# Kernel optimization log

Hardware: AMD Instinct MI355X
Metric: run time of the kernel (lower is better)

Reference implementation:

```python
import jax, jax.numpy as jnp
import numpy as np

OBS_DIM, ACTION_DIM, H, FC = 64, 100, 512, 256
IN_DIM = FC + ACTION_DIM


def setup_inputs() -> dict:
    key = jax.random.key(0)
    ks = jax.random.split(key, 10)
    s = lambda k, shp, fan: jax.random.normal(k, shp, jnp.float32) * (1.0 / np.sqrt(fan))
    return {
        "observations": jax.random.normal(ks[0], (32, 2048, OBS_DIM), jnp.float32),
        "actions": jax.random.uniform(ks[1], (32, 2048), jnp.float32),
        "W_obs": s(ks[2], (OBS_DIM, FC), OBS_DIM), "b_obs": jnp.zeros((FC,), jnp.float32),
        "W_act": s(ks[3], (1, ACTION_DIM), 1), "b_act": jnp.zeros((ACTION_DIM,), jnp.float32),
        "W_lstm": s(ks[4], (IN_DIM, 4 * H), IN_DIM),
        "U_lstm": s(ks[5], (H, 4 * H), H),
        "b_lstm": jnp.zeros((4 * H,), jnp.float32),
        "W_proj": s(ks[6], (H, ACTION_DIM), H), "b_proj": jnp.zeros((ACTION_DIM,), jnp.float32),
    }


def _lstm_seq(x, W, U, b):
    # x: [B, T, D] -> outputs [B, T, H]; keras LSTMCell default activations.
    B = x.shape[0]
    h0 = jnp.zeros((B, H), x.dtype)
    c0 = jnp.zeros((B, H), x.dtype)

    def step(carry, x_t):
        h, c = carry
        z = x_t @ W + h @ U + b  # [B, 4H]
        i, f, g, o = jnp.split(z, 4, axis=-1)
        i = jax.nn.sigmoid(i); f = jax.nn.sigmoid(f)
        g = jnp.tanh(g); o = jax.nn.sigmoid(o)
        c = f * c + i * g
        h = o * jnp.tanh(c)
        return (h, c), h

    _, hs = jax.lax.scan(step, (h0, c0), jnp.swapaxes(x, 0, 1))  # [T, B, H]
    return jnp.swapaxes(hs, 0, 1)


def reference(observations, actions, W_obs, b_obs, W_act, b_act,
              W_lstm, U_lstm, b_lstm, W_proj, b_proj):
    a = jax.nn.relu(actions[..., None] @ W_act + b_act)        # [B, T, A]
    ob = jax.nn.relu(observations @ W_obs + b_obs)             # [B, T, FC]
    x = jnp.concatenate([ob, a], axis=-1)                      # [B, T, FC+A]
    seq = _lstm_seq(x, W_lstm, U_lstm, b_lstm)                 # [B, T, H]
    logits = seq @ W_proj + b_proj                             # [B, T, A]
    pi = jax.nn.softmax(logits, axis=-1)
    # tf.math.argmax(logits) defaults to axis=0 (over batch), kept faithfully.
    argmax_actions = jnp.argmax(logits, axis=0)
    return pi, logits, argmax_actions
```

## Files before the change

### kernel.cpp

```cpp
#include <hip/hip_runtime.h>
#include <cstdint>
#include <cstddef>

#define B_   32
#define T_   2048
#define OBS_ 64
#define FC_  256
#define ACT_ 100
#define H_   512
#define TC_  128
#define NCH_ 16

typedef __attribute__((ext_vector_type(4))) unsigned int u32x4;
typedef __attribute__((ext_vector_type(8))) short bf16x8;
typedef __attribute__((ext_vector_type(4))) float f32x4;

static __device__ __forceinline__ bf16x8 as_b(u32x4 v){ union{u32x4 u; bf16x8 b;} x; x.u=v; return x.b; }
static __device__ __forceinline__ unsigned short f2bf(float f){
  unsigned int u = __builtin_bit_cast(unsigned int, f);
  return (unsigned short)((u + 0x7fffu + ((u>>16)&1u)) >> 16);
}
static __device__ __forceinline__ float bf2f(unsigned short s){
  unsigned int u = ((unsigned int)s) << 16;
  return __builtin_bit_cast(float, u);
}
static __device__ __forceinline__ void split3(float v, unsigned short& h, unsigned short& m, unsigned short& l){
  h = f2bf(v);
  float r1 = v - bf2f(h);
  m = f2bf(r1);
  float r2 = r1 - bf2f(m);
  l = f2bf(r2);
}
static __device__ __forceinline__ u32x4 pack8(const unsigned short* v){
  u32x4 r;
  r.x = (unsigned)v[0] | ((unsigned)v[1]<<16);
  r.y = (unsigned)v[2] | ((unsigned)v[3]<<16);
  r.z = (unsigned)v[4] | ((unsigned)v[5]<<16);
  r.w = (unsigned)v[6] | ((unsigned)v[7]<<16);
  return r;
}
static __device__ __forceinline__ u32x4 load_cohx4(const unsigned int* p){
  u32x4 r;
  asm volatile("global_load_dwordx4 %0, %1, off sc0 sc1"
               : "=&v"(r) : "v"(p) : "memory");
  return r;
}

static constexpr size_t XF_OFF    = 0;
static constexpr size_t XF_SZ     = (size_t)TC_*2*12*3*64*16;
static constexpr size_t WF_OFF    = XF_OFF + XF_SZ;
static constexpr size_t WF_SZ     = (size_t)32*4*28*3*64*16;
static constexpr size_t WPF_OFF   = WF_OFF + WF_SZ;
static constexpr size_t WPF_SZ    = (size_t)7*16*3*64*16;
static constexpr size_t ZX_OFF    = WPF_OFF + WPF_SZ;
static constexpr size_t ZX_SZ     = (size_t)TC_*2*2048*16*4;
static constexpr size_t HC01_OFF  = ZX_OFF + ZX_SZ;
static constexpr size_t HC01_SZ   = (size_t)TC_*2*16*512*4;
static constexpr size_t HC2_OFF   = HC01_OFF + HC01_SZ;
static constexpr size_t HC2_SZ    = (size_t)TC_*2*16*512*2;
static constexpr size_t HG_OFF    = HC2_OFF + HC2_SZ;
static constexpr size_t HG_SZ     = (size_t)3*2*16*2*256*4;
static constexpr size_t CST_OFF   = HG_OFF + HG_SZ;
static constexpr size_t CST_SZ    = (size_t)B_*H_*4;
static constexpr size_t CTR_OFF   = CST_OFF + CST_SZ;
static constexpr size_t CTR_SZ    = (size_t)2*T_*4;

__global__ __launch_bounds__(256) void k_prep_x(
    const float* __restrict__ obs, const float* __restrict__ act,
    const float* __restrict__ Wobs, const float* __restrict__ bobs,
    const float* __restrict__ Wact, const float* __restrict__ bact,
    u32x4* __restrict__ Xf, int tbase)
{
  __shared__ float Wl[64][257];
  __shared__ float ol[32][64];
  __shared__ float xr[32][256];
  __shared__ float al[32];
  __shared__ float wal[100], bal[100], bol[256];
  int tl = blockIdx.x; int t = tbase + tl; int tid = threadIdx.x;
  for (int i = tid; i < 64*256; i += 256) Wl[i>>8][i&255] = Wobs[i];
  for (int i = tid; i < 32*64; i += 256)
    ol[i>>6][i&63] = obs[((size_t)(i>>6)*T_ + t)*OBS_ + (i&63)];
  if (tid < 32) al[tid] = act[(size_t)tid*T_ + t];
  if (tid < 100) { wal[tid] = Wact[tid]; bal[tid] = bact[tid]; }
  bol[tid] = bobs[tid];
  __syncthreads();
  {
    int k = tid;
    double accd[32];
#pragma unroll
    for (int r = 0; r < 32; ++r) accd[r] = 0.0;
    for (int kc = 0; kc < 64; kc += 8) {
      float w[8];
#pragma unroll
      for (int q = 0; q < 8; ++q) w[q] = Wl[kc+q][k];
#pragma unroll
      for (int r = 0; r < 32; ++r) {
#pragma unroll
        for (int q = 0; q < 8; ++q) accd[r] += (double)w[q]*(double)ol[r][kc+q];
      }
    }
#pragma unroll
    for (int r = 0; r < 32; ++r) xr[r][k] = fmaxf((float)(accd[r] + (double)bol[k]), 0.f);
  }
  __syncthreads();
  int g = tid >> 6, l = tid & 63;
  int r = l & 15, sub = l >> 4;
  for (int p = g; p < 24; p += 4) {
    int bg = p / 12, kk = p % 12;
    int b = bg*16 + r;
    unsigned short vh[8], vm[8], vl[8];
#pragma unroll
    for (int j = 0; j < 8; ++j) {
      int k = kk*32 + sub*8 + j;
      float x;
      if (k < 256)      x = xr[b][k];
      else if (k < 356) {
        double tmp = (double)al[b]*(double)wal[k-256] + (double)bal[k-256];
        x = fmaxf((float)tmp, 0.f);
      } else            x = 0.f;
      split3(x, vh[j], vm[j], vl[j]);
    }
    size_t base = ((((size_t)tl*2 + bg)*12 + kk)*3)*64 + l;
    Xf[base]       = pack8(vh);
    Xf[base + 64]  = pack8(vm);
    Xf[base + 128] = pack8(vl);
  }
}

__global__ __launch_bounds__(256) void k_prep_w(
    const float* __restrict__ Wl, const float* __restrict__ Ul,
    unsigned short* __restrict__ Wf)
{
  size_t gid = (size_t)blockIdx.x*256 + threadIdx.x;
  if (gid >= (size_t)896*2048) return;
  int k = (int)(gid >> 11), oc = (int)(gid & 2047);
  float v = 0.f;
  if (k < 356) v = Wl[(size_t)k*2048 + oc];
  else if (k >= 384) v = Ul[(size_t)(k-384)*2048 + oc];
  unsigned short vh, vm, vlo;
  split3(v, vh, vm, vlo);
  int g = oc >> 9, hu = oc & 511;
  int hs = hu >> 4, wv = (hu >> 2) & 3, u = hu & 3;
  int cc = g*4 + u;
  int kk = k >> 5, sub = (k >> 3) & 3, j = k & 7;
  size_t e = ((((size_t)(hs*4 + wv)*28 + kk)*3 + 0)*64 + (sub*16 + cc))*8 + j;
  Wf[e]        = vh;
  Wf[e + 512]  = vm;
  Wf[e + 1024] = vlo;
}

__global__ __launch_bounds__(256) void k_prep_wp(
    const float* __restrict__ Wp, unsigned short* __restrict__ Wpf)
{
  int gid = blockIdx.x*256 + threadIdx.x;
  if (gid >= 512*112) return;
  int k = gid / 112, c = gid % 112;
  float v = (c < 100) ? Wp[(size_t)k*100 + c] : 0.f;
  unsigned short vh, vm, vlo;
  split3(v, vh, vm, vlo);
  int ct = c >> 4, cl = c & 15;
  int kk = k >> 5, sub = (k >> 3) & 3, j = k & 7;
  size_t e = (((size_t)(ct*16 + kk)*3 + 0)*64 + (sub*16 + cl))*8 + j;
  Wpf[e]        = vh;
  Wpf[e + 512]  = vm;
  Wpf[e + 1024] = vlo;
}

__global__ __launch_bounds__(256) void k_prep_zx(
    const u32x4* __restrict__ Xf, const u32x4* __restrict__ Wf,
    const float* __restrict__ blstm, float* __restrict__ zxT)
{
  int bid = blockIdx.x;
  int hq = bid & 7, bg = (bid >> 3) & 1, tl = bid >> 4;
  int tid = threadIdx.x;
  int v = tid >> 6, lane = tid & 63;
  int cc = lane & 15; int g = cc >> 2, u = cc & 3;
  int rbase = (lane >> 4) * 4;
  u32x4 xa[12][3];
  const u32x4* xp = Xf + (((size_t)tl*2 + bg)*12*3)*64 + lane;
#pragma unroll
  for (int f = 0; f < 12; ++f)
#pragma unroll
    for (int p = 0; p < 3; ++p) xa[f][p] = xp[(f*3+p)*64];
  for (int hi = 0; hi < 4; ++hi) {
    int hs = hq*4 + hi;
    const u32x4* bp = Wf + (((size_t)(hs*4 + v)*28)*3)*64 + lane;
    f32x4 a0={0,0,0,0},a1={0,0,0,0},a2={0,0,0,0},a3={0,0,0,0},a4={0,0,0,0},a5={0,0,0,0};
#pragma unroll
    for (int f = 0; f < 12; ++f) {
      u32x4 b0 = bp[(f*3+0)*64], b1 = bp[(f*3+1)*64], b2 = bp[(f*3+2)*64];
      a0 = __builtin_amdgcn_mfma_f32_16x16x32_bf16(as_b(xa[f][0]), as_b(b0), a0, 0,0,0);
      a1 = __builtin_amdgcn_mfma_f32_16x16x32_bf16(as_b(xa[f][0]), as_b(b1), a1, 0,0,0);
      a2 = __builtin_amdgcn_mfma_f32_16x16x32_bf16(as_b(xa[f][1]), as_b(b0), a2, 0,0,0);
      a3 = __builtin_amdgcn_mfma_f32_16x16x32_bf16(as_b(xa[f][0]), as_b(b2), a3, 0,0,0);
      a4 = __builtin_amdgcn_mfma_f32_16x16x32_bf16(as_b(xa[f][2]), as_b(b0), a4, 0,0,0);
      a5 = __builtin_amdgcn_mfma_f32_16x16x32_bf16(as_b(xa[f][1]), as_b(b1), a5, 0,0,0);
    }
    int oc = g*512 + hs*16 + v*4 + u;
    double bb = (double)blstm[oc];
    f32x4 st;
#pragma unroll
    for (int q = 0; q < 4; ++q) {
      double z = (((double)a3[q]+(double)a4[q])+(double)a5[q])
               + ((double)a1[q]+(double)a2[q]) + (double)a0[q] + bb;
      st[q] = (float)z;
    }
    *(f32x4*)(zxT + ((size_t)((size_t)(tl*2 + bg)*2048 + oc))*16 + rbase) = st;
  }
}

__global__ __launch_bounds__(256, 1) void k_rnn(
    const u32x4* __restrict__ Wf, const float* __restrict__ zxT,
    unsigned int* __restrict__ HC01, unsigned short* __restrict__ HC2,
    unsigned int* __restrict__ hg32, int* __restrict__ ctr,
    float* __restrict__ cstate, int tbase)
{
  int wg = blockIdx.x, bg = wg >> 5, hs = wg & 31;
  int tid = threadIdx.x, wv = tid >> 6, lane = tid & 63;
  int cc = lane & 15;
  int g = cc >> 2, u = cc & 3;
  int rbase = (lane >> 4) * 4;
  int U = hs*16 + wv*4 + u;
  u32x4 Breg[16][3];
  {
    const u32x4* bp = Wf + ((((size_t)(hs*4 + wv)*28) + 12)*3)*64 + lane;
#pragma unroll
    for (int f = 0; f < 16; ++f)
#pragma unroll
      for (int p = 0; p < 3; ++p) Breg[f][p] = bp[(f*3+p)*64];
#pragma unroll
    for (int f = 0; f < 16; ++f)
#pragma unroll
      for (int p = 0; p < 3; ++p) asm volatile("" : "+v"(Breg[f][p]));
  }
  float c[4];
#pragma unroll
  for (int q = 0; q < 4; ++q)
    c[q] = cstate[(size_t)(bg*16 + rbase + q)*512 + U];
  int Ue = hs*16 + wv*4 + (u & 2);
  int wkk = Ue >> 5, wsub = (Ue >> 3) & 3, wwrd = (Ue >> 1) & 3;

#pragma unroll 1
  for (int tl = 0; tl < TC_; ++tl) {
    int gt = tbase + tl;
    u32x4 hf0[16], hf1[16];
    {
      const unsigned int* hbase = hg32 + ((size_t)((gt+2)%3)*2 + bg)*16*2*256 + lane*4;
#pragma unroll
      for (int kk = 0; kk < 16; ++kk) {
        hf0[kk] = load_cohx4(hbase + (kk*2+0)*256);
        hf1[kk] = load_cohx4(hbase + (kk*2+1)*256);
      }
    }
    f32x4 zx = *(const f32x4*)(zxT + ((size_t)((size_t)(tl*2 + bg)*2048 + g*512 + U))*16 + rbase);
    asm volatile("s_waitcnt vmcnt(0)" ::: "memory");
    __builtin_amdgcn_sched_barrier(0);
    f32x4 a0={0,0,0,0},a1={0,0,0,0},a2={0,0,0,0},a3={0,0,0,0},a4={0,0,0,0};
#pragma unroll
    for (int kk = 0; kk < 16; ++kk) {
      a0 = __builtin_amdgcn_mfma_f32_16x16x32_bf16(as_b(hf0[kk]), as_b(Breg[kk][0]), a0, 0,0,0);
      a1 = __builtin_amdgcn_mfma_f32_16x16x32_bf16(as_b(hf0[kk]), as_b(Breg[kk][1]), a1, 0,0,0);
      a2 = __builtin_amdgcn_mfma_f32_16x16x32_bf16(as_b(hf1[kk]), as_b(Breg[kk][0]), a2, 0,0,0);
      a3 = __builtin_amdgcn_mfma_f32_16x16x32_bf16(as_b(hf0[kk]), as_b(Breg[kk][2]), a3, 0,0,0);
      a4 = __builtin_amdgcn_mfma_f32_16x16x32_bf16(as_b(hf1[kk]), as_b(Breg[kk][1]), a4, 0,0,0);
    }
    float hv[4];
#pragma unroll
    for (int q = 0; q < 4; ++q) {
      float z = (float)(((double)a3[q] + (double)a4[q])
                      + ((double)a1[q] + (double)a2[q]) + (double)a0[q]) + zx[q];
      float o0 = __shfl_xor(z, 4, 64);
      float e0 = (g & 1) ? o0 : z;
      float e1 = (g & 1) ? z  : o0;
      float p0 = __shfl_xor(e0, 8, 64);
      float p1 = __shfl_xor(e1, 8, 64);
      float zi = (g & 2) ? p0 : e0;
      float zf = (g & 2) ? p1 : e1;
      float zg = (g & 2) ? e0 : p0;
      float zo = (g & 2) ? e1 : p1;
      float i_ = 1.f/(1.f + expf(-zi));
      float f_ = 1.f/(1.f + expf(-zf));
      float g_ = tanhf(zg);
      float o_ = 1.f/(1.f + expf(-zo));
      c[q] = f_*c[q] + i_*g_;
      hv[q] = o_*tanhf(c[q]);
    }
    unsigned int* ringW = hg32 + ((size_t)(gt%3)*2 + bg)*16*2*256;
#pragma unroll
    for (int q = 0; q < 4; ++q) {
      float hq = hv[q];
      float hp = __shfl_xor(hq, 1, 64);
      unsigned short h0o = f2bf(hq);
      float r1 = hq - bf2f(h0o);
      unsigned short h1o = f2bf(r1);
      if (g == 0) {
        unsigned short h2o = f2bf(r1 - bf2f(h1o));
        size_t hcidx = ((size_t)(tl*2 + bg)*16 + rbase + q)*512 + U;
        HC01[hcidx] = (unsigned)h0o | ((unsigned)h1o << 16);
        HC2[hcidx]  = h2o;
        if (!(u & 1)) {
          unsigned short h0p = f2bf(hp);
          unsigned short h1p = f2bf(hp - bf2f(h0p));
          unsigned int w0 = (unsigned)h0o | ((unsigned)h0p << 16);
          unsigned int w1 = (unsigned)h1o | ((unsigned)h1p << 16);
          size_t d0 = ((size_t)wkk*2 + 0)*256 + (wsub*16 + rbase + q)*4 + wwrd;
          __hip_atomic_store(&ringW[d0],       w0, __ATOMIC_RELAXED, __HIP_MEMORY_SCOPE_AGENT);
          __hip_atomic_store(&ringW[d0 + 256], w1, __ATOMIC_RELAXED, __HIP_MEMORY_SCOPE_AGENT);
        }
      }
    }
    if (tl < TC_-1) {
      __syncthreads();
      if (tid == 0) {
        __hip_atomic_fetch_add(&ctr[bg*T_ + gt], 1, __ATOMIC_RELAXED, __HIP_MEMORY_SCOPE_AGENT);
        while (__hip_atomic_load(&ctr[bg*T_ + gt], __ATOMIC_RELAXED, __HIP_MEMORY_SCOPE_AGENT) < 32)
          __builtin_amdgcn_s_sleep(1);
      }
      __syncthreads();
    }
  }
#pragma unroll
  for (int q = 0; q < 4; ++q)
    if (g == 0) cstate[(size_t)(bg*16 + rbase + q)*512 + U] = c[q];
}

__global__ __launch_bounds__(256) void k_logits(
    const unsigned int* __restrict__ HC01, const unsigned short* __restrict__ HC2,
    const u32x4* __restrict__ Wpf,
    const float* __restrict__ bproj, float* __restrict__ out, int tbase)
{
  __shared__ float zl[16][120];
  int bid = blockIdx.x;
  int tl = bid >> 1, bg = bid & 1;
  int tid = threadIdx.x;
  int w = tid >> 6, lane = tid & 63;
  int row = lane & 15, koff = (lane >> 4) * 8;
  u32x4 a[16][3];
  {
    const unsigned int* h01 = HC01 + (((size_t)tl*2 + bg)*16 + row)*512 + koff;
    const unsigned short* h2p = HC2 + (((size_t)tl*2 + bg)*16 + row)*512 + koff;
#pragma unroll
    for (int kk = 0; kk < 16; ++kk) {
      u32x4 c0 = *(const u32x4*)(h01 + 32*kk);
      u32x4 c1 = *(const u32x4*)(h01 + 32*kk + 4);
      u32x4 p0, p1;
      p0.x = (c0.x & 0xffffu) | (c0.y << 16);
      p0.y = (c0.z & 0xffffu) | (c0.w << 16);
      p0.z = (c1.x & 0xffffu) | (c1.y << 16);
      p0.w = (c1.z & 0xffffu) | (c1.w << 16);
      p1.x = (c0.x >> 16) | (c0.y & 0xffff0000u);
      p1.y = (c0.z >> 16) | (c0.w & 0xffff0000u);
      p1.z = (c1.x >> 16) | (c1.y & 0xffff0000u);
      p1.w = (c1.z >> 16) | (c1.w & 0xffff0000u);
      a[kk][0] = p0;
      a[kk][1] = p1;
      a[kk][2] = *(const u32x4*)(h2p + 32*kk);
    }
  }
  for (int ct = w; ct < 7; ct += 4) {
    f32x4 c0 = {0,0,0,0}, c1 = {0,0,0,0}, c2 = {0,0,0,0};
    f32x4 c3 = {0,0,0,0}, c4 = {0,0,0,0}, c5 = {0,0,0,0};
    const u32x4* bp2 = Wpf + ((size_t)ct*16*3)*64 + lane;
#pragma unroll
    for (int kk = 0; kk < 16; ++kk) {
      u32x4 b0 = bp2[(kk*3+0)*64], b1 = bp2[(kk*3+1)*64], b2 = bp2[(kk*3+2)*64];
      c0 = __builtin_amdgcn_mfma_f32_16x16x32_bf16(as_b(a[kk][0]), as_b(b0), c0, 0,0,0);
      c1 = __builtin_amdgcn_mfma_f32_16x16x32_bf16(as_b(a[kk][0]), as_b(b1), c1, 0,0,0);
      c2 = __builtin_amdgcn_mfma_f32_16x16x32_bf16(as_b(a[kk][1]), as_b(b0), c2, 0,0,0);
      c3 = __builtin_amdgcn_mfma_f32_16x16x32_bf16(as_b(a[kk][0]), as_b(b2), c3, 0,0,0);
      c4 = __builtin_amdgcn_mfma_f32_16x16x32_bf16(as_b(a[kk][2]), as_b(b0), c4, 0,0,0);
      c5 = __builtin_amdgcn_mfma_f32_16x16x32_bf16(as_b(a[kk][1]), as_b(b1), c5, 0,0,0);
    }
    int col = ct*16 + (lane & 15);
    float bv = (col < 100) ? bproj[col] : 0.f;
#pragma unroll
    for (int q = 0; q < 4; ++q) {
      double z = (((double)c3[q] + (double)c4[q]) + (double)c5[q])
               + ((double)c1[q] + (double)c2[q]) + (double)c0[q] + (double)bv;
      if (col < 120) zl[(lane>>4)*4 + q][col] = (float)z;
    }
  }
  __syncthreads();
  int srow = tid >> 4, l16 = tid & 15;
  float vv[7];
  float m = -1e30f;
#pragma unroll
  for (int k2 = 0; k2 < 7; ++k2) {
    int col = l16 + 16*k2;
    vv[k2] = (col < 100) ? zl[srow][col] : -1e30f;
    m = fmaxf(m, vv[k2]);
  }
#pragma unroll
  for (int d = 1; d < 16; d <<= 1) m = fmaxf(m, __shfl_xor(m, d, 64));
  float s = 0.f; float ek[7];
#pragma unroll
  for (int k2 = 0; k2 < 7; ++k2) {
    int col = l16 + 16*k2;
    ek[k2] = (col < 100) ? expf(vv[k2] - m) : 0.f;
    s += ek[k2];
  }
#pragma unroll
  for (int d = 1; d < 16; d <<= 1) s += __shfl_xor(s, d, 64);
  int t = tbase + tl; int b = bg*16 + srow;
  float* piout = out;
  float* lgout = out + 6553600ull;
#pragma unroll
  for (int k2 = 0; k2 < 7; ++k2) {
    int col = l16 + 16*k2;
    if (col < 100) {
      size_t idx = ((size_t)b*T_ + t)*100 + col;
      lgout[idx] = vv[k2];
      piout[idx] = ek[k2] / s;
    }
  }
}

__global__ __launch_bounds__(128) void k_argmax(
    const float* __restrict__ lg, float* __restrict__ outA)
{
  int t = blockIdx.x, j = threadIdx.x;
  if (j >= 100) return;
  float best = lg[(size_t)t*100 + j];
  int bi = 0;
  for (int b = 1; b < 32; ++b) {
    float v = lg[((size_t)b*T_ + t)*100 + j];
    if (v > best) { best = v; bi = b; }
  }
  outA[(size_t)t*100 + j] = (float)bi;
}

extern "C" void kernel_launch(void* const* d_in, const int* in_sizes, int n_in,
                              void* d_out, int out_size, void* d_ws, size_t ws_size,
                              hipStream_t stream) {
  const float* obs  = (const float*)d_in[0];
  const float* act  = (const float*)d_in[1];
  const float* Wobs = (const float*)d_in[2];
  const float* bobs = (const float*)d_in[3];
  const float* Wact = (const float*)d_in[4];
  const float* bact = (const float*)d_in[5];
  const float* Wl   = (const float*)d_in[6];
  const float* Ul   = (const float*)d_in[7];
  const float* bl   = (const float*)d_in[8];
  const float* Wp   = (const float*)d_in[9];
  const float* bp   = (const float*)d_in[10];
  char* ws = (char*)d_ws;
  u32x4* Xf             = (u32x4*)(ws + XF_OFF);
  unsigned short* WfS   = (unsigned short*)(ws + WF_OFF);
  unsigned short* WpfS  = (unsigned short*)(ws + WPF_OFF);
  float* zxT            = (float*)(ws + ZX_OFF);
  unsigned int* HC01    = (unsigned int*)(ws + HC01_OFF);
  unsigned short* HC2   = (unsigned short*)(ws + HC2_OFF);
  unsigned int* hg32    = (unsigned int*)(ws + HG_OFF);
  float* cstate         = (float*)(ws + CST_OFF);
  int* ctr              = (int*)(ws + CTR_OFF);
  float* out = (float*)d_out;

  hipMemsetAsync(ws + HG_OFF, 0, HG_SZ + CST_SZ + CTR_SZ, stream);
  k_prep_w<<<7168, 256, 0, stream>>>(Wl, Ul, WfS);
  k_prep_wp<<<(512*112 + 255)/256, 256, 0, stream>>>(Wp, WpfS);
  for (int ch = 0; ch < NCH_; ++ch) {
    int tb = ch * TC_;
    k_prep_x<<<TC_, 256, 0, stream>>>(obs, act, Wobs, bobs, Wact, bact, Xf, tb);
    k_prep_zx<<<TC_*2*8, 256, 0, stream>>>((const u32x4*)Xf, (const u32x4*)WfS, bl, zxT);
    k_rnn<<<64, 256, 0, stream>>>((const u32x4*)WfS, zxT, HC01, HC2,
                                  hg32, ctr, cstate, tb);
    k_logits<<<TC_*2, 256, 0, stream>>>(HC01, HC2, (const u32x4*)WpfS, bp, out, tb);
  }
  k_argmax<<<T_, 128, 0, stream>>>(out + 6553600ull, out + 13107200ull);
}
```

Before: 12.99 ms.

## Replace per-step atomic barrier with per-wave flags and drop third bf16 split

The recurrent kernel no longer uses a workgroup syncthreads plus a global atomic counter spin at each timestep. Each wave now publishes a per-wave ready flag, and consumers poll all 128 flags of the previous step with coherent loads before reading h. Precision is also reduced: the three-term bf16 split becomes two terms in both the recurrent and logits matmuls, dropping the HC2 buffer and cutting MFMA counts. Double accumulation in the recurrence becomes float. This shortens the serial critical path per step but risks accuracy loss and depends on memory ordering being correct.

```diff
diff --git a/kernel.cpp b/kernel.cpp
--- a/kernel.cpp
+++ b/kernel.cpp
@@ -56,14 +56,12 @@
 static constexpr size_t ZX_SZ     = (size_t)TC_*2*2048*16*4;
 static constexpr size_t HC01_OFF  = ZX_OFF + ZX_SZ;
 static constexpr size_t HC01_SZ   = (size_t)TC_*2*16*512*4;
-static constexpr size_t HC2_OFF   = HC01_OFF + HC01_SZ;
-static constexpr size_t HC2_SZ    = (size_t)TC_*2*16*512*2;
-static constexpr size_t HG_OFF    = HC2_OFF + HC2_SZ;
+static constexpr size_t HG_OFF    = HC01_OFF + HC01_SZ;
 static constexpr size_t HG_SZ     = (size_t)3*2*16*2*256*4;
 static constexpr size_t CST_OFF   = HG_OFF + HG_SZ;
 static constexpr size_t CST_SZ    = (size_t)B_*H_*4;
-static constexpr size_t CTR_OFF   = CST_OFF + CST_SZ;
-static constexpr size_t CTR_SZ    = (size_t)2*T_*4;
+static constexpr size_t FLG_OFF   = CST_OFF + CST_SZ;
+static constexpr size_t FLG_SZ    = (size_t)T_*2*128*4;
 
 __global__ __launch_bounds__(256) void k_prep_x(
     const float* __restrict__ obs, const float* __restrict__ act,
@@ -211,8 +209,8 @@
 
 __global__ __launch_bounds__(256, 1) void k_rnn(
     const u32x4* __restrict__ Wf, const float* __restrict__ zxT,
-    unsigned int* __restrict__ HC01, unsigned short* __restrict__ HC2,
-    unsigned int* __restrict__ hg32, int* __restrict__ ctr,
+    unsigned int* __restrict__ HC01,
+    unsigned int* __restrict__ hg32, unsigned int* __restrict__ flags,
     float* __restrict__ cstate, int tbase)
 {
   int wg = blockIdx.x, bg = wg >> 5, hs = wg & 31;
@@ -221,17 +219,13 @@
   int g = cc >> 2, u = cc & 3;
   int rbase = (lane >> 4) * 4;
   int U = hs*16 + wv*4 + u;
-  u32x4 Breg[16][3];
+  u32x4 Breg[16][2];
   {
     const u32x4* bp = Wf + ((((size_t)(hs*4 + wv)*28) + 12)*3)*64 + lane;
 #pragma unroll
     for (int f = 0; f < 16; ++f)
 #pragma unroll
-      for (int p = 0; p < 3; ++p) Breg[f][p] = bp[(f*3+p)*64];
-#pragma unroll
-    for (int f = 0; f < 16; ++f)
-#pragma unroll
-      for (int p = 0; p < 3; ++p) asm volatile("" : "+v"(Breg[f][p]));
+      for (int p = 0; p < 2; ++p) Breg[f][p] = bp[(f*3+p)*64];
   }
   float c[4];
 #pragma unroll
@@ -239,10 +233,25 @@
     c[q] = cstate[(size_t)(bg*16 + rbase + q)*512 + U];
   int Ue = hs*16 + wv*4 + (u & 2);
   int wkk = Ue >> 5, wsub = (Ue >> 3) & 3, wwrd = (Ue >> 1) & 3;
+  int fslot = hs*4 + wv;
 
 #pragma unroll 1
   for (int tl = 0; tl < TC_; ++tl) {
     int gt = tbase + tl;
+#pragma unroll
+    for (int f = 0; f < 16; ++f)
+      asm volatile("" : "+v"(Breg[f][0]), "+v"(Breg[f][1]));
+    if (gt > 0) {
+      const unsigned int* fb = flags + ((size_t)(gt-1)*2 + bg)*128;
+      unsigned int f0, f1;
+      do {
+        asm volatile("global_load_dword %0, %2, off sc0 sc1\n\t"
+                     "global_load_dword %1, %3, off sc0 sc1\n\t"
+                     "s_waitcnt vmcnt(0)"
+                     : "=&v"(f0), "=&v"(f1)
+                     : "v"(fb + lane), "v"(fb + 64 + lane) : "memory");
+      } while (!__all(f0 && f1));
+    }
     u32x4 hf0[16], hf1[16];
     {
       const unsigned int* hbase = hg32 + ((size_t)((gt+2)%3)*2 + bg)*16*2*256 + lane*4;
@@ -255,20 +264,17 @@
     f32x4 zx = *(const f32x4*)(zxT + ((size_t)((size_t)(tl*2 + bg)*2048 + g*512 + U))*16 + rbase);
     asm volatile("s_waitcnt vmcnt(0)" ::: "memory");
     __builtin_amdgcn_sched_barrier(0);
-    f32x4 a0={0,0,0,0},a1={0,0,0,0},a2={0,0,0,0},a3={0,0,0,0},a4={0,0,0,0};
+    f32x4 a0={0,0,0,0},a1={0,0,0,0},a2={0,0,0,0};
 #pragma unroll
     for (int kk = 0; kk < 16; ++kk) {
       a0 = __builtin_amdgcn_mfma_f32_16x16x32_bf16(as_b(hf0[kk]), as_b(Breg[kk][0]), a0, 0,0,0);
       a1 = __builtin_amdgcn_mfma_f32_16x16x32_bf16(as_b(hf0[kk]), as_b(Breg[kk][1]), a1, 0,0,0);
       a2 = __builtin_amdgcn_mfma_f32_16x16x32_bf16(as_b(hf1[kk]), as_b(Breg[kk][0]), a2, 0,0,0);
-      a3 = __builtin_amdgcn_mfma_f32_16x16x32_bf16(as_b(hf0[kk]), as_b(Breg[kk][2]), a3, 0,0,0);
-      a4 = __builtin_amdgcn_mfma_f32_16x16x32_bf16(as_b(hf1[kk]), as_b(Breg[kk][1]), a4, 0,0,0);
     }
     float hv[4];
 #pragma unroll
     for (int q = 0; q < 4; ++q) {
-      float z = (float)(((double)a3[q] + (double)a4[q])
-                      + ((double)a1[q] + (double)a2[q]) + (double)a0[q]) + zx[q];
+      float z = (a1[q] + a2[q]) + a0[q] + zx[q];
       float o0 = __shfl_xor(z, 4, 64);
       float e0 = (g & 1) ? o0 : z;
       float e1 = (g & 1) ? z  : o0;
@@ -291,13 +297,10 @@
       float hq = hv[q];
       float hp = __shfl_xor(hq, 1, 64);
       unsigned short h0o = f2bf(hq);
-      float r1 = hq - bf2f(h0o);
-      unsigned short h1o = f2bf(r1);
+      unsigned short h1o = f2bf(hq - bf2f(h0o));
       if (g == 0) {
-        unsigned short h2o = f2bf(r1 - bf2f(h1o));
         size_t hcidx = ((size_t)(tl*2 + bg)*16 + rbase + q)*512 + U;
         HC01[hcidx] = (unsigned)h0o | ((unsigned)h1o << 16);
-        HC2[hcidx]  = h2o;
         if (!(u & 1)) {
           unsigned short h0p = f2bf(hp);
           unsigned short h1p = f2bf(hp - bf2f(h0p));
@@ -309,14 +312,10 @@
         }
       }
     }
-    if (tl < TC_-1) {
-      __syncthreads();
-      if (tid == 0) {
-        __hip_atomic_fetch_add(&ctr[bg*T_ + gt], 1, __ATOMIC_RELAXED, __HIP_MEMORY_SCOPE_AGENT);
-        while (__hip_atomic_load(&ctr[bg*T_ + gt], __ATOMIC_RELAXED, __HIP_MEMORY_SCOPE_AGENT) < 32)
-          __builtin_amdgcn_s_sleep(1);
-      }
-      __syncthreads();
+    asm volatile("s_waitcnt vmcnt(0)" ::: "memory");
+    if (lane == 0) {
+      unsigned int* fp = flags + ((size_t)gt*2 + bg)*128 + fslot;
+      __hip_atomic_store(fp, 1u, __ATOMIC_RELAXED, __HIP_MEMORY_SCOPE_AGENT);
     }
   }
 #pragma unroll
@@ -325,7 +324,7 @@
 }
 
 __global__ __launch_bounds__(256) void k_logits(
-    const unsigned int* __restrict__ HC01, const unsigned short* __restrict__ HC2,
+    const unsigned int* __restrict__ HC01,
     const u32x4* __restrict__ Wpf,
     const float* __restrict__ bproj, float* __restrict__ out, int tbase)
 {
@@ -335,10 +334,9 @@
   int tid = threadIdx.x;
   int w = tid >> 6, lane = tid & 63;
   int row = lane & 15, koff = (lane >> 4) * 8;
-  u32x4 a[16][3];
+  u32x4 a[16][2];
   {
     const unsigned int* h01 = HC01 + (((size_t)tl*2 + bg)*16 + row)*512 + koff;
-    const unsigned short* h2p = HC2 + (((size_t)tl*2 + bg)*16 + row)*512 + koff;
 #pragma unroll
     for (int kk = 0; kk < 16; ++kk) {
       u32x4 c0 = *(const u32x4*)(h01 + 32*kk);
@@ -354,29 +352,23 @@
       p1.w = (c1.z >> 16) | (c1.w & 0xffff0000u);
       a[kk][0] = p0;
       a[kk][1] = p1;
-      a[kk][2] = *(const u32x4*)(h2p + 32*kk);
     }
   }
   for (int ct = w; ct < 7; ct += 4) {
     f32x4 c0 = {0,0,0,0}, c1 = {0,0,0,0}, c2 = {0,0,0,0};
-    f32x4 c3 = {0,0,0,0}, c4 = {0,0,0,0}, c5 = {0,0,0,0};
     const u32x4* bp2 = Wpf + ((size_t)ct*16*3)*64 + lane;
 #pragma unroll
     for (int kk = 0; kk < 16; ++kk) {
-      u32x4 b0 = bp2[(kk*3+0)*64], b1 = bp2[(kk*3+1)*64], b2 = bp2[(kk*3+2)*64];
+      u32x4 b0 = bp2[(kk*3+0)*64], b1 = bp2[(kk*3+1)*64];
       c0 = __builtin_amdgcn_mfma_f32_16x16x32_bf16(as_b(a[kk][0]), as_b(b0), c0, 0,0,0);
       c1 = __builtin_amdgcn_mfma_f32_16x16x32_bf16(as_b(a[kk][0]), as_b(b1), c1, 0,0,0);
       c2 = __builtin_amdgcn_mfma_f32_16x16x32_bf16(as_b(a[kk][1]), as_b(b0), c2, 0,0,0);
-      c3 = __builtin_amdgcn_mfma_f32_16x16x32_bf16(as_b(a[kk][0]), as_b(b2), c3, 0,0,0);
-      c4 = __builtin_amdgcn_mfma_f32_16x16x32_bf16(as_b(a[kk][2]), as_b(b0), c4, 0,0,0);
-      c5 = __builtin_amdgcn_mfma_f32_16x16x32_bf16(as_b(a[kk][1]), as_b(b1), c5, 0,0,0);
     }
     int col = ct*16 + (lane & 15);
     float bv = (col < 100) ? bproj[col] : 0.f;
 #pragma unroll
     for (int q = 0; q < 4; ++q) {
-      double z = (((double)c3[q] + (double)c4[q]) + (double)c5[q])
-               + ((double)c1[q] + (double)c2[q]) + (double)c0[q] + (double)bv;
+      double z = ((double)c1[q] + (double)c2[q]) + (double)c0[q] + (double)bv;
       if (col < 120) zl[(lane>>4)*4 + q][col] = (float)z;
     }
   }
@@ -449,22 +441,21 @@
   unsigned short* WpfS  = (unsigned short*)(ws + WPF_OFF);
   float* zxT            = (float*)(ws + ZX_OFF);
   unsigned int* HC01    = (unsigned int*)(ws + HC01_OFF);
-  unsigned short* HC2   = (unsigned short*)(ws + HC2_OFF);
   unsigned int* hg32    = (unsigned int*)(ws + HG_OFF);
   float* cstate         = (float*)(ws + CST_OFF);
-  int* ctr              = (int*)(ws + CTR_OFF);
+  unsigned int* flags   = (unsigned int*)(ws + FLG_OFF);
   float* out = (float*)d_out;
 
-  hipMemsetAsync(ws + HG_OFF, 0, HG_SZ + CST_SZ + CTR_SZ, stream);
+  hipMemsetAsync(ws + HG_OFF, 0, HG_SZ + CST_SZ + FLG_SZ, stream);
   k_prep_w<<<7168, 256, 0, stream>>>(Wl, Ul, WfS);
   k_prep_wp<<<(512*112 + 255)/256, 256, 0, stream>>>(Wp, WpfS);
   for (int ch = 0; ch < NCH_; ++ch) {
     int tb = ch * TC_;
     k_prep_x<<<TC_, 256, 0, stream>>>(obs, act, Wobs, bobs, Wact, bact, Xf, tb);
     k_prep_zx<<<TC_*2*8, 256, 0, stream>>>((const u32x4*)Xf, (const u32x4*)WfS, bl, zxT);
-    k_rnn<<<64, 256, 0, stream>>>((const u32x4*)WfS, zxT, HC01, HC2,
-                                  hg32, ctr, cstate, tb);
-    k_logits<<<TC_*2, 256, 0, stream>>>(HC01, HC2, (const u32x4*)WpfS, bp, out, tb);
+    k_rnn<<<64, 256, 0, stream>>>((const u32x4*)WfS, zxT, HC01,
+                                  hg32, flags, cstate, tb);
+    k_logits<<<TC_*2, 256, 0, stream>>>(HC01, (const u32x4*)WpfS, bp, out, tb);
   }
   k_argmax<<<T_, 128, 0, stream>>>(out + 6553600ull, out + 13107200ull);
 }
```

New measurement: 15.72 ms. +21.0%, slower.
